# Optimization experiments

Measured on AMD Instinct MI355X. Metric: run time of the kernel, lower is better.

Reference implementation:

```python
import jax, jax.numpy as jnp
import numpy as np

PATCH = 3
PAD = (PATCH - 1) // 2
WEIGHT = 100.0
EPS = 1e-9


def _extract_patches(fm):
    # fm: (C, H, W) -> (H*W, C*9) row i*W+j is the reflect-padded 3x3 patch at (i, j)
    C, H, W = fm.shape
    fm_pad = jnp.pad(fm, ((0, 0), (PAD, PAD), (PAD, PAD)), mode='reflect')
    shifts = [fm_pad[:, dh:dh + H, dw:dw + W] for dh in range(PATCH) for dw in range(PATCH)]
    p = jnp.stack(shifts, axis=0)            # (9, C, H, W)
    return p.reshape(PATCH * PATCH * C, H * W).T  # (HW, 9C)


def _match_fm(content_fm, style_fm):
    # content_fm, style_fm: (1, C, H, W); returns matched style fm (1,C,H,W) and idx (2,H,W)
    C, H, W = content_fm.shape[1:]
    cp = _extract_patches(content_fm[0])     # (HW, 9C) content patches (conv kernels)
    sp = _extract_patches(style_fm[0])       # (HW, 9C) style patches (conv sliding windows)
    c_norm = jnp.sqrt(jnp.sum(cp * cp, axis=1))  # kernel_norm per content location
    s_norm = jnp.sqrt(jnp.sum(sp * sp, axis=1))  # style_fm_norm per style location
    score = cp @ sp.T                            # (HW, HW) cross-correlation
    score = score / (c_norm[:, None] * s_norm[None, :] + EPS)
    idx = jnp.argmax(score, axis=1)              # flat argmax == torch.argmax on (H,W) map
    style_flat = style_fm[0].reshape(C, H * W)
    corr = style_flat[:, idx].reshape(1, C, H, W)  # gather matched style pixels
    corr_idx = jnp.stack([idx // W, idx % W], axis=0).reshape(2, H, W)
    return corr, corr_idx


def _masked_gram(fm, mask_flat, mask_sum):
    # fm: (1, C, H, W), mask_flat: (HW,) -> (C, C) gram of masked fm / sum(mask)
    C = fm.shape[1]
    f = fm[0].reshape(C, -1) * mask_flat[None, :]
    return (f @ f.T) / mask_sum


def setup_inputs() -> dict:
    key = jax.random.key(0)
    k1, k2, k3, k4 = jax.random.split(key, 4)
    B, C, H, W = 1, 512, 64, 64
    return {
        'content_fm': jax.random.normal(k1, (B, C, H, W), dtype=jnp.float32),
        'style_fm': jax.random.normal(k2, (B, C, H, W), dtype=jnp.float32),
        'input_fm': jax.random.normal(k3, (B, C, H, W), dtype=jnp.float32),
        'mask': jax.random.uniform(k4, (B, 1, H, W), dtype=jnp.float32),
    }


def reference(content_fm, style_fm, input_fm, mask):
    H, W = content_fm.shape[2:]
    mask_flat = mask[0, 0].reshape(H * W)
    mask_sum = jnp.sum(mask)
    # capture_style_ref: patch-match style fm to content fm, build target gram
    corr_fm, _ = _match_fm(content_fm, style_fm)
    target_gram = _masked_gram(corr_fm, mask_flat, mask_sum)
    # loss mode: masked gram of current image fm vs target, MSE (mean) * weight
    G = _masked_gram(input_fm, mask_flat, mask_sum)
    loss = jnp.mean((G - target_gram) ** 2) * WEIGHT
    return loss
```

## Files before the change

kernel.cpp:

```cpp
#include <hip/hip_runtime.h>

static constexpr int C  = 512;
static constexpr int P  = 4096;
static constexpr int CC = 262144;

typedef _Float16 half8  __attribute__((ext_vector_type(8)));
typedef _Float16 half2v __attribute__((ext_vector_type(2)));
typedef float    f32x4  __attribute__((ext_vector_type(4)));

__device__ __forceinline__ int refl(int q) { return q < 0 ? 1 : (q > 63 ? 62 : q); }

__device__ __forceinline__ void g2l16(const void* g, const void* l) {
    __builtin_amdgcn_global_load_lds((const __attribute__((address_space(1))) unsigned int*)g,
                                     (__attribute__((address_space(3))) unsigned int*)l, 16, 0, 0);
}

__global__ void k_init(float* __restrict__ small) {
    int e = blockIdx.x * 256 + threadIdx.x;
    if (e < 4096) small[e] = 0.0f;
    if (e == 4096) small[8193] = 0.0f;
}

__global__ __launch_bounds__(256) void k_prep(const float* __restrict__ content, const float* __restrict__ style,
                                              _Float16* __restrict__ Ah, _Float16* __restrict__ Bh,
                                              float* __restrict__ sqn_s) {
    __shared__ float T[64][65];
    const int p0 = (blockIdx.x & 63) * 64, c0 = (blockIdx.x >> 6) * 64;
    const int pl = threadIdx.x & 63, cq = threadIdx.x >> 6;
    const int cl2 = threadIdx.x & 63, pq = threadIdx.x >> 6;

    #pragma unroll
    for (int r = 0; r < 16; ++r) {
        int cl = cq + r * 4;
        T[cl][pl] = content[(size_t)(c0 + cl) * P + p0 + pl];
    }
    __syncthreads();
    #pragma unroll
    for (int r = 0; r < 16; ++r) {
        int pl2 = pq + r * 4;
        Ah[(size_t)(p0 + pl2) * C + c0 + cl2] = (_Float16)T[cl2][pl2];
    }
    __syncthreads();

    float sq = 0.f;
    #pragma unroll
    for (int r = 0; r < 16; ++r) {
        int cl = cq + r * 4;
        float v = style[(size_t)(c0 + cl) * P + p0 + pl];
        T[cl][pl] = v;
        sq += v * v;
    }
    atomicAdd(&sqn_s[p0 + pl], sq);
    __syncthreads();
    #pragma unroll
    for (int r = 0; r < 16; ++r) {
        int pl2 = pq + r * 4;
        Bh[(size_t)(p0 + pl2) * C + c0 + cl2] = (_Float16)T[cl2][pl2];
    }
}

__global__ void k_pnorm(const float* __restrict__ sqn_s, const float* __restrict__ mask,
                        float* __restrict__ inv_sn, float* __restrict__ msum) {
    int p = blockIdx.x * 256 + threadIdx.x;
    int i = p >> 6, j = p & 63;
    float s2 = 0.f;
    #pragma unroll
    for (int dh = -1; dh <= 1; ++dh) {
        int ih = refl(i + dh);
        #pragma unroll
        for (int dw = -1; dw <= 1; ++dw)
            s2 += sqn_s[ih * 64 + refl(j + dw)];
    }
    inv_sn[p] = 1.0f / sqrtf(s2);

    if (blockIdx.x == 0) {
        __shared__ float red[256];
        float s = 0.f;
        for (int e = threadIdx.x; e < P; e += 256) s += mask[e];
        red[threadIdx.x] = s;
        __syncthreads();
        for (int t = 128; t > 0; t >>= 1) {
            if (threadIdx.x < t) red[threadIdx.x] += red[threadIdx.x + t];
            __syncthreads();
        }
        if (threadIdx.x == 0) msum[0] = red[0];
    }
}

__global__ __launch_bounds__(256) void k_gemm16(const _Float16* __restrict__ Ah,
                                                const _Float16* __restrict__ Bh,
                                                _Float16* __restrict__ D0h) {
    __shared__ _Float16 As[128 * 64];
    __shared__ _Float16 Bs[128 * 64];
    const int tid = threadIdx.x;
    const int wave = tid >> 6, lane = tid & 63;
    const int wr = wave >> 1, wc = wave & 1;
    const int quad = lane >> 4, l15 = lane & 15;
    const int i0 = blockIdx.y * 128, j0 = blockIdx.x * 128;

    int mloc[4], goff[4];
    #pragma unroll
    for (int c2 = 0; c2 < 4; ++c2) {
        int m = wave * 32 + c2 * 8 + (lane >> 3);
        mloc[c2] = m;
        goff[c2] = ((lane & 7) ^ (m & 7)) * 8;
    }

    int aoff[4][2], boff[4][2];
    #pragma unroll
    for (int mi = 0; mi < 4; ++mi) {
        int m = wr * 64 + mi * 16 + l15;
        int n = wc * 64 + mi * 16 + l15;
        #pragma unroll
        for (int kh = 0; kh < 2; ++kh) {
            aoff[mi][kh] = m * 64 + ((quad + kh * 4) ^ (m & 7)) * 8;
            boff[mi][kh] = n * 64 + ((quad + kh * 4) ^ (n & 7)) * 8;
        }
    }

    f32x4 acc[4][4] = {};

    for (int kk = 0; kk < C; kk += 64) {
        __syncthreads();
        #pragma unroll
        for (int c2 = 0; c2 < 4; ++c2) {
            g2l16(Ah + (size_t)(i0 + mloc[c2]) * C + kk + goff[c2], As + (wave * 32 + c2 * 8) * 64);
            g2l16(Bh + (size_t)(j0 + mloc[c2]) * C + kk + goff[c2], Bs + (wave * 32 + c2 * 8) * 64);
        }
        __syncthreads();
        half8 af[2][4], bf[2][4];
        #pragma unroll
        for (int kh = 0; kh < 2; ++kh)
            #pragma unroll
            for (int mi = 0; mi < 4; ++mi) {
                af[kh][mi] = *(const half8*)(As + aoff[mi][kh]);
                bf[kh][mi] = *(const half8*)(Bs + boff[mi][kh]);
            }
        #pragma unroll
        for (int kh = 0; kh < 2; ++kh)
            #pragma unroll
            for (int mi = 0; mi < 4; ++mi)
                #pragma unroll
                for (int ni = 0; ni < 4; ++ni)
                    acc[mi][ni] = __builtin_amdgcn_mfma_f32_16x16x32_f16(af[kh][mi], bf[kh][ni], acc[mi][ni], 0, 0, 0);
    }

    #pragma unroll
    for (int mi = 0; mi < 4; ++mi) {
        int row = i0 + wr * 64 + mi * 16 + quad * 4;
        #pragma unroll
        for (int ni = 0; ni < 4; ++ni) {
            int col = j0 + wc * 64 + ni * 16 + l15;
            #pragma unroll
            for (int r = 0; r < 4; ++r)
                D0h[(size_t)(row + r) * P + col] = (_Float16)acc[mi][ni][r];
        }
    }
}

__global__ __launch_bounds__(256) void k_argmax(const _Float16* __restrict__ D0h,
                                                const float* __restrict__ inv_sn,
                                                int* __restrict__ idxOut) {
    const int i = blockIdx.x;
    const int ih = i >> 6, iw = i & 63;
    const int wave = threadIdx.x >> 6, l = threadIdx.x & 63, l15 = l & 15;
    int rb[9];
    #pragma unroll
    for (int t = 0; t < 9; ++t) {
        int dh = t / 3 - 1, dw = t % 3 - 1;
        rb[t] = (refl(ih + dh) * 64 + refl(iw + dw)) * P;
    }
    float best = -1e30f;
    int bidx = 0;
    #pragma unroll
    for (int s = 0; s < 4; ++s) {
        const int ws = wave * 4 + s;
        const int j0 = ws * 256 + l * 4;
        const int jh = j0 >> 6;
        const int jw0 = l15 * 4;
        const int rs0 = (jh == 0) ? 1 : jh - 1;
        const int rs2 = (jh == 63) ? 62 : jh + 1;
        const int cb[3] = { rs0 * 64 + jw0, jh * 64 + jw0, rs2 * 64 + jw0 };

        float f[4] = {0.f, 0.f, 0.f, 0.f};
        #pragma unroll
        for (int dh = 0; dh < 3; ++dh) {
            const uint2 vm = *(const uint2*)(D0h + rb[dh * 3 + 0] + cb[dh]);
            const uint2 vc = *(const uint2*)(D0h + rb[dh * 3 + 1] + cb[dh]);
            const uint2 vp = *(const uint2*)(D0h + rb[dh * 3 + 2] + cb[dh]);
            unsigned prev_hi = (unsigned)__shfl((int)vm.y, l - 1);
            unsigned next_lo = (unsigned)__shfl((int)vp.x, l + 1);
            unsigned left16  = ((l15 == 0) ? vm.x : prev_hi) >> 16;
            unsigned right16 = ((l15 == 15) ? vp.y : next_lo) & 0xffffu;
            unsigned wl0 = left16 | (vm.x << 16);
            unsigned wl1 = (vm.x >> 16) | (vm.y << 16);
            unsigned wr0 = (vp.x >> 16) | (vp.y << 16);
            unsigned wr1 = (vp.y >> 16) | (right16 << 16);
            half2v a0 = __builtin_bit_cast(half2v, wl0), a1 = __builtin_bit_cast(half2v, wl1);
            half2v b0 = __builtin_bit_cast(half2v, vc.x), b1 = __builtin_bit_cast(half2v, vc.y);
            half2v c0 = __builtin_bit_cast(half2v, wr0), c1 = __builtin_bit_cast(half2v, wr1);
            f[0] += (float)a0[0] + (float)b0[0] + (float)c0[0];
            f[1] += (float)a0[1] + (float)b0[1] + (float)c0[1];
            f[2] += (float)a1[0] + (float)b1[0] + (float)c1[0];
            f[3] += (float)a1[1] + (float)b1[1] + (float)c1[1];
        }
        const float4 is = *(const float4*)(inv_sn + j0);
        float v0 = f[0] * is.x, v1 = f[1] * is.y, v2 = f[2] * is.z, v3 = f[3] * is.w;
        if (v0 > best) { best = v0; bidx = j0; }
        if (v1 > best) { best = v1; bidx = j0 + 1; }
        if (v2 > best) { best = v2; bidx = j0 + 2; }
        if (v3 > best) { best = v3; bidx = j0 + 3; }
    }
    __shared__ float bv[256];
    __shared__ int   bi[256];
    bv[threadIdx.x] = best;
    bi[threadIdx.x] = bidx;
    __syncthreads();
    for (int t = 128; t > 0; t >>= 1) {
        if (threadIdx.x < t) {
            float ov = bv[threadIdx.x + t];
            int   oi = bi[threadIdx.x + t];
            if (ov > bv[threadIdx.x] || (ov == bv[threadIdx.x] && oi < bi[threadIdx.x])) {
                bv[threadIdx.x] = ov;
                bi[threadIdx.x] = oi;
            }
        }
        __syncthreads();
    }
    if (threadIdx.x == 0) idxOut[i] = bi[0];
}

__global__ void k_build(const float* __restrict__ style, const float* __restrict__ input,
                        const float* __restrict__ mask, const int* __restrict__ idx,
                        _Float16* __restrict__ fc, _Float16* __restrict__ fg) {
    int t = blockIdx.x * 256 + threadIdx.x;
    int e0 = t * 8;
    int p0 = e0 & (P - 1), c = e0 >> 12;
    half8 vg, vc;
    #pragma unroll
    for (int u = 0; u < 8; ++u) {
        float m = mask[p0 + u];
        vg[u] = (_Float16)(input[e0 + u] * m);
        vc[u] = (_Float16)(style[(c << 12) + idx[p0 + u]] * m);
    }
    *(half8*)(fg + e0) = vg;
    *(half8*)(fc + e0) = vc;
}

__global__ __launch_bounds__(256) void k_gram(const _Float16* __restrict__ fg,
                                              const _Float16* __restrict__ fc,
                                              float* __restrict__ part) {
    const int z = blockIdx.z;
    const int p0 = z * 256;
    const int wave = threadIdx.x >> 6, lane = threadIdx.x & 63;
    const int wr = wave >> 1, wc = wave & 1, quad = lane >> 4, l15 = lane & 15;
    const int a0 = blockIdx.y * 128 + wr * 64, b0 = blockIdx.x * 128 + wc * 64;

    f32x4 accg[4][4] = {};
    f32x4 accc[4][4] = {};
    for (int ks = 0; ks < 256; ks += 32) {
        int kbase = p0 + ks + quad * 8;
        half8 af[4], bf[4];
        #pragma unroll
        for (int mi = 0; mi < 4; ++mi) af[mi] = *(const half8*)(fg + (size_t)(a0 + mi * 16 + l15) * P + kbase);
        #pragma unroll
        for (int ni = 0; ni < 4; ++ni) bf[ni] = *(const half8*)(fg + (size_t)(b0 + ni * 16 + l15) * P + kbase);
        #pragma unroll
        for (int mi = 0; mi < 4; ++mi)
            #pragma unroll
            for (int ni = 0; ni < 4; ++ni)
                accg[mi][ni] = __builtin_amdgcn_mfma_f32_16x16x32_f16(af[mi], bf[ni], accg[mi][ni], 0, 0, 0);
        #pragma unroll
        for (int mi = 0; mi < 4; ++mi) af[mi] = *(const half8*)(fc + (size_t)(a0 + mi * 16 + l15) * P + kbase);
        #pragma unroll
        for (int ni = 0; ni < 4; ++ni) bf[ni] = *(const half8*)(fc + (size_t)(b0 + ni * 16 + l15) * P + kbase);
        #pragma unroll
        for (int mi = 0; mi < 4; ++mi)
            #pragma unroll
            for (int ni = 0; ni < 4; ++ni)
                accc[mi][ni] = __builtin_amdgcn_mfma_f32_16x16x32_f16(af[mi], bf[ni], accc[mi][ni], 0, 0, 0);
    }
    #pragma unroll
    for (int mi = 0; mi < 4; ++mi)
        #pragma unroll
        for (int ni = 0; ni < 4; ++ni)
            #pragma unroll
            for (int r = 0; r < 4; ++r)
                part[(size_t)z * CC + (size_t)(a0 + mi * 16 + quad * 4 + r) * C + b0 + ni * 16 + l15]
                    = accg[mi][ni][r] - accc[mi][ni][r];
}

__global__ void k_loss(const float* __restrict__ part, float* __restrict__ acc) {
    int e = blockIdx.x * 256 + threadIdx.x;
    float d = 0.f;
    #pragma unroll
    for (int z = 0; z < 16; ++z) d += part[(size_t)z * CC + e];
    __shared__ float red[256];
    red[threadIdx.x] = d * d;
    __syncthreads();
    for (int t = 128; t > 0; t >>= 1) {
        if (threadIdx.x < t) red[threadIdx.x] += red[threadIdx.x + t];
        __syncthreads();
    }
    if (threadIdx.x == 0) atomicAdd(acc, red[0]);
}

__global__ void k_final(const float* __restrict__ msum, const float* __restrict__ acc,
                        float* __restrict__ out) {
    float m = msum[0];
    out[0] = acc[0] * 100.0f / (m * m * 262144.0f);
}

extern "C" void kernel_launch(void* const* d_in, const int* in_sizes, int n_in,
                              void* d_out, int out_size, void* d_ws, size_t ws_size,
                              hipStream_t stream) {
    (void)in_sizes; (void)n_in; (void)out_size; (void)ws_size;
    const float* content = (const float*)d_in[0];
    const float* style   = (const float*)d_in[1];
    const float* input   = (const float*)d_in[2];
    const float* mask    = (const float*)d_in[3];

    char* ws = (char*)d_ws;
    _Float16* D0h  = (_Float16*)ws;
    float*    part = (float*)ws;
    _Float16* Ah   = (_Float16*)(ws + (32u << 20));
    _Float16* Bh   = (_Float16*)(ws + (36u << 20));
    _Float16* fg_h = (_Float16*)(ws + (40u << 20));
    _Float16* fc_h = (_Float16*)(ws + (44u << 20));
    float*    small = (float*)(ws + (48u << 20));
    float* sqn_s  = small;
    float* inv_sn = small + 4096;
    float* msum   = small + 8192;
    float* acc    = small + 8193;
    int*   idx    = (int*)(small + 8194);
    float* out = (float*)d_out;

    k_init  <<<17, 256, 0, stream>>>(small);
    k_prep  <<<512, 256, 0, stream>>>(content, style, Ah, Bh, sqn_s);
    k_pnorm <<<16, 256, 0, stream>>>(sqn_s, mask, inv_sn, msum);
    k_gemm16<<<dim3(32, 32), 256, 0, stream>>>(Ah, Bh, D0h);
    k_argmax<<<4096, 256, 0, stream>>>(D0h, inv_sn, idx);
    k_build <<<1024, 256, 0, stream>>>(style, input, mask, idx, fc_h, fg_h);
    k_gram  <<<dim3(4, 4, 16), 256, 0, stream>>>(fg_h, fc_h, part);
    k_loss  <<<1024, 256, 0, stream>>>(part, acc);
    k_final <<<1, 1, 0, stream>>>(msum, acc, out);
}
```

Measured before the change: 173.8 us.

## Tile argmax over 2x2 content pixels and fold small kernels via last-block counters

```diff
diff --git a/kernel.cpp b/kernel.cpp
--- a/kernel.cpp
+++ b/kernel.cpp
@@ -15,15 +15,22 @@
                                      (__attribute__((address_space(3))) unsigned int*)l, 16, 0, 0);
 }
 
+
 __global__ void k_init(float* __restrict__ small) {
     int e = blockIdx.x * 256 + threadIdx.x;
     if (e < 4096) small[e] = 0.0f;
-    if (e == 4096) small[8193] = 0.0f;
+    if (e == 0) {
+        small[8193] = 0.0f;
+        ((unsigned*)small)[8194] = 0u;
+        ((unsigned*)small)[8195] = 0u;
+    }
 }
 
 __global__ __launch_bounds__(256) void k_prep(const float* __restrict__ content, const float* __restrict__ style,
+                                              const float* __restrict__ mask,
                                               _Float16* __restrict__ Ah, _Float16* __restrict__ Bh,
-                                              float* __restrict__ sqn_s) {
+                                              float* __restrict__ sqn_s, float* __restrict__ inv_sn,
+                                              float* __restrict__ msum, unsigned* __restrict__ cnt) {
     __shared__ float T[64][65];
     const int p0 = (blockIdx.x & 63) * 64, c0 = (blockIdx.x >> 6) * 64;
     const int pl = threadIdx.x & 63, cq = threadIdx.x >> 6;
@@ -57,26 +64,32 @@
         int pl2 = pq + r * 4;
         Bh[(size_t)(p0 + pl2) * C + c0 + cl2] = (_Float16)T[cl2][pl2];
     }
-}
-
-__global__ void k_pnorm(const float* __restrict__ sqn_s, const float* __restrict__ mask,
-                        float* __restrict__ inv_sn, float* __restrict__ msum) {
-    int p = blockIdx.x * 256 + threadIdx.x;
-    int i = p >> 6, j = p & 63;
-    float s2 = 0.f;
-    #pragma unroll
-    for (int dh = -1; dh <= 1; ++dh) {
-        int ih = refl(i + dh);
-        #pragma unroll
-        for (int dw = -1; dw <= 1; ++dw)
-            s2 += sqn_s[ih * 64 + refl(j + dw)];
-    }
-    inv_sn[p] = 1.0f / sqrtf(s2);
-
-    if (blockIdx.x == 0) {
+
+    __threadfence();
+    __syncthreads();
+    __shared__ unsigned lastv;
+    if (threadIdx.x == 0) lastv = atomicAdd(cnt, 1);
+    __syncthreads();
+    if (lastv == 511) {
+        __shared__ float sqs[4096];
+        for (int r = threadIdx.x; r < 4096; r += 256)
+            sqs[r] = __hip_atomic_load(&sqn_s[r], __ATOMIC_RELAXED, __HIP_MEMORY_SCOPE_AGENT);
+        __syncthreads();
+        for (int r = threadIdx.x; r < 4096; r += 256) {
+            int i = r >> 6, j = r & 63;
+            float s2 = 0.f;
+            #pragma unroll
+            for (int dh = -1; dh <= 1; ++dh) {
+                int ih = refl(i + dh);
+                #pragma unroll
+                for (int dw = -1; dw <= 1; ++dw)
+                    s2 += sqs[ih * 64 + refl(j + dw)];
+            }
+            inv_sn[r] = 1.0f / sqrtf(s2);
+        }
         __shared__ float red[256];
         float s = 0.f;
-        for (int e = threadIdx.x; e < P; e += 256) s += mask[e];
+        for (int e = threadIdx.x; e < 4096; e += 256) s += mask[e];
         red[threadIdx.x] = s;
         __syncthreads();
         for (int t = 128; t > 0; t >>= 1) {
@@ -161,17 +174,25 @@
 __global__ __launch_bounds__(256) void k_argmax(const _Float16* __restrict__ D0h,
                                                 const float* __restrict__ inv_sn,
                                                 int* __restrict__ idxOut) {
-    const int i = blockIdx.x;
-    const int ih = i >> 6, iw = i & 63;
+    const int T = blockIdx.x;
+    const int ih0 = (T >> 5) * 2, iw0 = (T & 31) * 2;
     const int wave = threadIdx.x >> 6, l = threadIdx.x & 63, l15 = l & 15;
-    int rb[9];
-    #pragma unroll
-    for (int t = 0; t < 9; ++t) {
-        int dh = t / 3 - 1, dw = t % 3 - 1;
-        rb[t] = (refl(ih + dh) * 64 + refl(iw + dw)) * P;
-    }
-    float best = -1e30f;
-    int bidx = 0;
+
+    int rh[4], rw[4];
+    rh[0] = refl(ih0 - 1); rh[1] = ih0; rh[2] = ih0 + 1; rh[3] = refl(ih0 + 2);
+    rw[0] = refl(iw0 - 1); rw[1] = iw0; rw[2] = iw0 + 1; rw[3] = refl(iw0 + 2);
+    int rb[3][2][4];
+    #pragma unroll
+    for (int d = 0; d < 3; ++d)
+        #pragma unroll
+        for (int di = 0; di < 2; ++di)
+            #pragma unroll
+            for (int k = 0; k < 4; ++k)
+                rb[d][di][k] = (rh[di + d] * 64 + rw[k]) * P;
+
+    float best[2][2] = {{-1e30f, -1e30f}, {-1e30f, -1e30f}};
+    int   bidx[2][2] = {{0, 0}, {0, 0}};
+
     #pragma unroll
     for (int s = 0; s < 4; ++s) {
         const int ws = wave * 4 + s;
@@ -182,52 +203,73 @@
         const int rs2 = (jh == 63) ? 62 : jh + 1;
         const int cb[3] = { rs0 * 64 + jw0, jh * 64 + jw0, rs2 * 64 + jw0 };
 
-        float f[4] = {0.f, 0.f, 0.f, 0.f};
-        #pragma unroll
-        for (int dh = 0; dh < 3; ++dh) {
-            const uint2 vm = *(const uint2*)(D0h + rb[dh * 3 + 0] + cb[dh]);
-            const uint2 vc = *(const uint2*)(D0h + rb[dh * 3 + 1] + cb[dh]);
-            const uint2 vp = *(const uint2*)(D0h + rb[dh * 3 + 2] + cb[dh]);
-            unsigned prev_hi = (unsigned)__shfl((int)vm.y, l - 1);
-            unsigned next_lo = (unsigned)__shfl((int)vp.x, l + 1);
-            unsigned left16  = ((l15 == 0) ? vm.x : prev_hi) >> 16;
-            unsigned right16 = ((l15 == 15) ? vp.y : next_lo) & 0xffffu;
-            unsigned wl0 = left16 | (vm.x << 16);
-            unsigned wl1 = (vm.x >> 16) | (vm.y << 16);
-            unsigned wr0 = (vp.x >> 16) | (vp.y << 16);
-            unsigned wr1 = (vp.y >> 16) | (right16 << 16);
-            half2v a0 = __builtin_bit_cast(half2v, wl0), a1 = __builtin_bit_cast(half2v, wl1);
-            half2v b0 = __builtin_bit_cast(half2v, vc.x), b1 = __builtin_bit_cast(half2v, vc.y);
-            half2v c0 = __builtin_bit_cast(half2v, wr0), c1 = __builtin_bit_cast(half2v, wr1);
-            f[0] += (float)a0[0] + (float)b0[0] + (float)c0[0];
-            f[1] += (float)a0[1] + (float)b0[1] + (float)c0[1];
-            f[2] += (float)a1[0] + (float)b1[0] + (float)c1[0];
-            f[3] += (float)a1[1] + (float)b1[1] + (float)c1[1];
+        float f[2][2][4] = {};
+        #pragma unroll
+        for (int d = 0; d < 3; ++d) {
+            #pragma unroll
+            for (int di = 0; di < 2; ++di) {
+                uint2 u[4];
+                #pragma unroll
+                for (int k = 0; k < 4; ++k)
+                    u[k] = *(const uint2*)(D0h + rb[d][di][k] + cb[d]);
+                #pragma unroll
+                for (int dj = 0; dj < 2; ++dj) {
+                    const uint2 A = u[dj], Bc = u[dj + 1], Cc = u[dj + 2];
+                    unsigned prev_hi = (unsigned)__shfl((int)A.y, l - 1);
+                    unsigned next_lo = (unsigned)__shfl((int)Cc.x, l + 1);
+                    unsigned left16  = ((l15 == 0) ? A.x : prev_hi) >> 16;
+                    unsigned right16 = ((l15 == 15) ? Cc.y : next_lo) & 0xffffu;
+                    unsigned wl0 = left16 | (A.x << 16);
+                    unsigned wl1 = (A.x >> 16) | (A.y << 16);
+                    unsigned wr0 = (Cc.x >> 16) | (Cc.y << 16);
+                    unsigned wr1 = (Cc.y >> 16) | (right16 << 16);
+                    half2v a0 = __builtin_bit_cast(half2v, wl0), a1 = __builtin_bit_cast(half2v, wl1);
+                    half2v b0 = __builtin_bit_cast(half2v, Bc.x), b1 = __builtin_bit_cast(half2v, Bc.y);
+                    half2v c0 = __builtin_bit_cast(half2v, wr0), c1 = __builtin_bit_cast(half2v, wr1);
+                    f[di][dj][0] += (float)a0[0] + (float)b0[0] + (float)c0[0];
+                    f[di][dj][1] += (float)a0[1] + (float)b0[1] + (float)c0[1];
+                    f[di][dj][2] += (float)a1[0] + (float)b1[0] + (float)c1[0];
+                    f[di][dj][3] += (float)a1[1] + (float)b1[1] + (float)c1[1];
+                }
+            }
         }
         const float4 is = *(const float4*)(inv_sn + j0);
-        float v0 = f[0] * is.x, v1 = f[1] * is.y, v2 = f[2] * is.z, v3 = f[3] * is.w;
-        if (v0 > best) { best = v0; bidx = j0; }
-        if (v1 > best) { best = v1; bidx = j0 + 1; }
-        if (v2 > best) { best = v2; bidx = j0 + 2; }
-        if (v3 > best) { best = v3; bidx = j0 + 3; }
-    }
+        #pragma unroll
+        for (int di = 0; di < 2; ++di)
+            #pragma unroll
+            for (int dj = 0; dj < 2; ++dj) {
+                float v0 = f[di][dj][0] * is.x, v1 = f[di][dj][1] * is.y;
+                float v2 = f[di][dj][2] * is.z, v3 = f[di][dj][3] * is.w;
+                if (v0 > best[di][dj]) { best[di][dj] = v0; bidx[di][dj] = j0; }
+                if (v1 > best[di][dj]) { best[di][dj] = v1; bidx[di][dj] = j0 + 1; }
+                if (v2 > best[di][dj]) { best[di][dj] = v2; bidx[di][dj] = j0 + 2; }
+                if (v3 > best[di][dj]) { best[di][dj] = v3; bidx[di][dj] = j0 + 3; }
+            }
+    }
+
     __shared__ float bv[256];
     __shared__ int   bi[256];
-    bv[threadIdx.x] = best;
-    bi[threadIdx.x] = bidx;
-    __syncthreads();
-    for (int t = 128; t > 0; t >>= 1) {
-        if (threadIdx.x < t) {
-            float ov = bv[threadIdx.x + t];
-            int   oi = bi[threadIdx.x + t];
-            if (ov > bv[threadIdx.x] || (ov == bv[threadIdx.x] && oi < bi[threadIdx.x])) {
-                bv[threadIdx.x] = ov;
-                bi[threadIdx.x] = oi;
-            }
-        }
-        __syncthreads();
-    }
-    if (threadIdx.x == 0) idxOut[i] = bi[0];
+    #pragma unroll
+    for (int di = 0; di < 2; ++di)
+        #pragma unroll
+        for (int dj = 0; dj < 2; ++dj) {
+            __syncthreads();
+            bv[threadIdx.x] = best[di][dj];
+            bi[threadIdx.x] = bidx[di][dj];
+            __syncthreads();
+            for (int t = 128; t > 0; t >>= 1) {
+                if (threadIdx.x < t) {
+                    float ov = bv[threadIdx.x + t];
+                    int   oi = bi[threadIdx.x + t];
+                    if (ov > bv[threadIdx.x] || (ov == bv[threadIdx.x] && oi < bi[threadIdx.x])) {
+                        bv[threadIdx.x] = ov;
+                        bi[threadIdx.x] = oi;
+                    }
+                }
+                __syncthreads();
+            }
+            if (threadIdx.x == 0) idxOut[(ih0 + di) * 64 + iw0 + dj] = bi[0];
+        }
 }
 
 __global__ void k_build(const float* __restrict__ style, const float* __restrict__ input,
@@ -290,7 +332,9 @@
                     = accg[mi][ni][r] - accc[mi][ni][r];
 }
 
-__global__ void k_loss(const float* __restrict__ part, float* __restrict__ acc) {
+__global__ void k_loss(const float* __restrict__ part, float* __restrict__ acc,
+                       unsigned* __restrict__ cnt, const float* __restrict__ msum,
+                       float* __restrict__ out) {
     int e = blockIdx.x * 256 + threadIdx.x;
     float d = 0.f;
     #pragma unroll
@@ -302,13 +346,16 @@
         if (threadIdx.x < t) red[threadIdx.x] += red[threadIdx.x + t];
         __syncthreads();
     }
-    if (threadIdx.x == 0) atomicAdd(acc, red[0]);
-}
-
-__global__ void k_final(const float* __restrict__ msum, const float* __restrict__ acc,
-                        float* __restrict__ out) {
-    float m = msum[0];
-    out[0] = acc[0] * 100.0f / (m * m * 262144.0f);
+    if (threadIdx.x == 0) {
+        atomicAdd(acc, red[0]);
+        __threadfence();
+        unsigned old = atomicAdd(cnt, 1);
+        if (old == 1023) {
+            float a = __hip_atomic_load(acc, __ATOMIC_RELAXED, __HIP_MEMORY_SCOPE_AGENT);
+            float m = msum[0];
+            out[0] = a * 100.0f / (m * m * 262144.0f);
+        }
+    }
 }
 
 extern "C" void kernel_launch(void* const* d_in, const int* in_sizes, int n_in,
@@ -328,20 +375,20 @@
     _Float16* fg_h = (_Float16*)(ws + (40u << 20));
     _Float16* fc_h = (_Float16*)(ws + (44u << 20));
     float*    small = (float*)(ws + (48u << 20));
-    float* sqn_s  = small;
-    float* inv_sn = small + 4096;
-    float* msum   = small + 8192;
-    float* acc    = small + 8193;
-    int*   idx    = (int*)(small + 8194);
+    float*    sqn_s  = small;
+    float*    inv_sn = small + 4096;
+    float*    msum   = small + 8192;
+    float*    acc    = small + 8193;
+    unsigned* cntp   = (unsigned*)(small + 8194);
+    unsigned* cntl   = (unsigned*)(small + 8195);
+    int*      idx    = (int*)(small + 8196);
     float* out = (float*)d_out;
 
-    k_init  <<<17, 256, 0, stream>>>(small);
-    k_prep  <<<512, 256, 0, stream>>>(content, style, Ah, Bh, sqn_s);
-    k_pnorm <<<16, 256, 0, stream>>>(sqn_s, mask, inv_sn, msum);
+    k_init  <<<16, 256, 0, stream>>>(small);
+    k_prep  <<<512, 256, 0, stream>>>(content, style, mask, Ah, Bh, sqn_s, inv_sn, msum, cntp);
     k_gemm16<<<dim3(32, 32), 256, 0, stream>>>(Ah, Bh, D0h);
-    k_argmax<<<4096, 256, 0, stream>>>(D0h, inv_sn, idx);
+    k_argmax<<<1024, 256, 0, stream>>>(D0h, inv_sn, idx);
     k_build <<<1024, 256, 0, stream>>>(style, input, mask, idx, fc_h, fg_h);
     k_gram  <<<dim3(4, 4, 16), 256, 0, stream>>>(fg_h, fc_h, part);
-    k_loss  <<<1024, 256, 0, stream>>>(part, acc);
-    k_final <<<1, 1, 0, stream>>>(msum, acc, out);
-}
+    k_loss  <<<1024, 256, 0, stream>>>(part, acc, cntl, msum, out);
+}
```

New measurement: 259.4 us. 1.49x slower.

## Fuse horizontal 3-tap patch sum into GEMM epilogue, simplify argmax to 3 taps

Applied to the files above, without the earlier changes.

```diff
diff --git a/kernel.cpp b/kernel.cpp
--- a/kernel.cpp
+++ b/kernel.cpp
@@ -18,7 +18,7 @@
 __global__ void k_init(float* __restrict__ small) {
     int e = blockIdx.x * 256 + threadIdx.x;
     if (e < 4096) small[e] = 0.0f;
-    if (e == 4096) small[8193] = 0.0f;
+    if (e == 0) small[8193] = 0.0f;
 }
 
 __global__ __launch_bounds__(256) void k_prep(const float* __restrict__ content, const float* __restrict__ style,
@@ -89,9 +89,10 @@
 
 __global__ __launch_bounds__(256) void k_gemm16(const _Float16* __restrict__ Ah,
                                                 const _Float16* __restrict__ Bh,
-                                                _Float16* __restrict__ D0h) {
-    __shared__ _Float16 As[128 * 64];
-    __shared__ _Float16 Bs[128 * 64];
+                                                _Float16* __restrict__ Eo) {
+    __shared__ _Float16 SH[16640];
+    _Float16* As = SH;
+    _Float16* Bs = SH + 8192;
     const int tid = threadIdx.x;
     const int wave = tid >> 6, lane = tid & 63;
     const int wr = wave >> 1, wc = wave & 1;
@@ -145,72 +146,78 @@
                     acc[mi][ni] = __builtin_amdgcn_mfma_f32_16x16x32_f16(af[kh][mi], bf[kh][ni], acc[mi][ni], 0, 0, 0);
     }
 
+    __syncthreads();
     #pragma unroll
     for (int mi = 0; mi < 4; ++mi) {
-        int row = i0 + wr * 64 + mi * 16 + quad * 4;
+        int row = wr * 64 + mi * 16 + quad * 4;
         #pragma unroll
         for (int ni = 0; ni < 4; ++ni) {
-            int col = j0 + wc * 64 + ni * 16 + l15;
+            int col = wc * 64 + ni * 16 + l15;
             #pragma unroll
             for (int r = 0; r < 4; ++r)
-                D0h[(size_t)(row + r) * P + col] = (_Float16)acc[mi][ni][r];
-        }
-    }
-}
-
-__global__ __launch_bounds__(256) void k_argmax(const _Float16* __restrict__ D0h,
+                SH[(row + r) * 130 + col] = (_Float16)acc[mi][ni][r];
+        }
+    }
+    __syncthreads();
+
+    const int er  = tid >> 1;
+    const int ec0 = (tid & 1) << 6;
+    const int aw = er & 63;
+    const int rm = (er & 64) | (aw == 0 ? 1 : aw - 1);
+    const int rp = (er & 64) | (aw == 63 ? 62 : aw + 1);
+    _Float16* outRow = Eo + (size_t)(i0 + er) * P + j0 + ec0;
+    #pragma unroll
+    for (int cc = 0; cc < 64; cc += 8) {
+        half8 ev;
+        #pragma unroll
+        for (int u = 0; u < 8; ++u) {
+            int c = ec0 + cc + u;
+            int cw = c & 63;
+            int cm = (c & 64) | (cw == 0 ? 1 : cw - 1);
+            int cp = (c & 64) | (cw == 63 ? 62 : cw + 1);
+            ev[u] = (_Float16)((float)SH[rm * 130 + cm] + (float)SH[er * 130 + c] + (float)SH[rp * 130 + cp]);
+        }
+        *(half8*)(outRow + cc) = ev;
+    }
+}
+
+__global__ __launch_bounds__(256) void k_argmax(const _Float16* __restrict__ E,
                                                 const float* __restrict__ inv_sn,
                                                 int* __restrict__ idxOut) {
     const int i = blockIdx.x;
     const int ih = i >> 6, iw = i & 63;
     const int wave = threadIdx.x >> 6, l = threadIdx.x & 63, l15 = l & 15;
-    int rb[9];
-    #pragma unroll
-    for (int t = 0; t < 9; ++t) {
-        int dh = t / 3 - 1, dw = t % 3 - 1;
-        rb[t] = (refl(ih + dh) * 64 + refl(iw + dw)) * P;
-    }
+    size_t rb0 = (size_t)(refl(ih - 1) * 64 + iw) * P;
+    size_t rb1 = (size_t)(ih * 64 + iw) * P;
+    size_t rb2 = (size_t)(refl(ih + 1) * 64 + iw) * P;
+
     float best = -1e30f;
     int bidx = 0;
     #pragma unroll
     for (int s = 0; s < 4; ++s) {
-        const int ws = wave * 4 + s;
-        const int j0 = ws * 256 + l * 4;
-        const int jh = j0 >> 6;
-        const int jw0 = l15 * 4;
-        const int rs0 = (jh == 0) ? 1 : jh - 1;
-        const int rs2 = (jh == 63) ? 62 : jh + 1;
-        const int cb[3] = { rs0 * 64 + jw0, jh * 64 + jw0, rs2 * 64 + jw0 };
-
-        float f[4] = {0.f, 0.f, 0.f, 0.f};
-        #pragma unroll
-        for (int dh = 0; dh < 3; ++dh) {
-            const uint2 vm = *(const uint2*)(D0h + rb[dh * 3 + 0] + cb[dh]);
-            const uint2 vc = *(const uint2*)(D0h + rb[dh * 3 + 1] + cb[dh]);
-            const uint2 vp = *(const uint2*)(D0h + rb[dh * 3 + 2] + cb[dh]);
-            unsigned prev_hi = (unsigned)__shfl((int)vm.y, l - 1);
-            unsigned next_lo = (unsigned)__shfl((int)vp.x, l + 1);
-            unsigned left16  = ((l15 == 0) ? vm.x : prev_hi) >> 16;
-            unsigned right16 = ((l15 == 15) ? vp.y : next_lo) & 0xffffu;
-            unsigned wl0 = left16 | (vm.x << 16);
-            unsigned wl1 = (vm.x >> 16) | (vm.y << 16);
-            unsigned wr0 = (vp.x >> 16) | (vp.y << 16);
-            unsigned wr1 = (vp.y >> 16) | (right16 << 16);
-            half2v a0 = __builtin_bit_cast(half2v, wl0), a1 = __builtin_bit_cast(half2v, wl1);
-            half2v b0 = __builtin_bit_cast(half2v, vc.x), b1 = __builtin_bit_cast(half2v, vc.y);
-            half2v c0 = __builtin_bit_cast(half2v, wr0), c1 = __builtin_bit_cast(half2v, wr1);
-            f[0] += (float)a0[0] + (float)b0[0] + (float)c0[0];
-            f[1] += (float)a0[1] + (float)b0[1] + (float)c0[1];
-            f[2] += (float)a1[0] + (float)b1[0] + (float)c1[0];
-            f[3] += (float)a1[1] + (float)b1[1] + (float)c1[1];
-        }
+        const int j0 = (wave * 4 + s) * 256 + l * 4;
+        const int jh = j0 >> 6, jw0 = l15 * 4;
+        const int cb0 = ((jh == 0) ? 1 : jh - 1) * 64 + jw0;
+        const int cb1 = jh * 64 + jw0;
+        const int cb2 = ((jh == 63) ? 62 : jh + 1) * 64 + jw0;
+        uint2 u0 = *(const uint2*)(E + rb0 + cb0);
+        uint2 u1 = *(const uint2*)(E + rb1 + cb1);
+        uint2 u2 = *(const uint2*)(E + rb2 + cb2);
+        half2v a0 = __builtin_bit_cast(half2v, u0.x), a1 = __builtin_bit_cast(half2v, u0.y);
+        half2v b0 = __builtin_bit_cast(half2v, u1.x), b1 = __builtin_bit_cast(half2v, u1.y);
+        half2v c0 = __builtin_bit_cast(half2v, u2.x), c1 = __builtin_bit_cast(half2v, u2.y);
+        float f0 = (float)a0[0] + (float)b0[0] + (float)c0[0];
+        float f1 = (float)a0[1] + (float)b0[1] + (float)c0[1];
+        float f2 = (float)a1[0] + (float)b1[0] + (float)c1[0];
+        float f3 = (float)a1[1] + (float)b1[1] + (float)c1[1];
         const float4 is = *(const float4*)(inv_sn + j0);
-        float v0 = f[0] * is.x, v1 = f[1] * is.y, v2 = f[2] * is.z, v3 = f[3] * is.w;
+        float v0 = f0 * is.x, v1 = f1 * is.y, v2 = f2 * is.z, v3 = f3 * is.w;
         if (v0 > best) { best = v0; bidx = j0; }
         if (v1 > best) { best = v1; bidx = j0 + 1; }
         if (v2 > best) { best = v2; bidx = j0 + 2; }
         if (v3 > best) { best = v3; bidx = j0 + 3; }
     }
+
     __shared__ float bv[256];
     __shared__ int   bi[256];
     bv[threadIdx.x] = best;
@@ -321,7 +328,7 @@
     const float* mask    = (const float*)d_in[3];
 
     char* ws = (char*)d_ws;
-    _Float16* D0h  = (_Float16*)ws;
+    _Float16* Eb   = (_Float16*)ws;
     float*    part = (float*)ws;
     _Float16* Ah   = (_Float16*)(ws + (32u << 20));
     _Float16* Bh   = (_Float16*)(ws + (36u << 20));
@@ -335,11 +342,11 @@
     int*   idx    = (int*)(small + 8194);
     float* out = (float*)d_out;
 
-    k_init  <<<17, 256, 0, stream>>>(small);
+    k_init  <<<16, 256, 0, stream>>>(small);
     k_prep  <<<512, 256, 0, stream>>>(content, style, Ah, Bh, sqn_s);
     k_pnorm <<<16, 256, 0, stream>>>(sqn_s, mask, inv_sn, msum);
-    k_gemm16<<<dim3(32, 32), 256, 0, stream>>>(Ah, Bh, D0h);
-    k_argmax<<<4096, 256, 0, stream>>>(D0h, inv_sn, idx);
+    k_gemm16<<<dim3(32, 32), 256, 0, stream>>>(Ah, Bh, Eb);
+    k_argmax<<<4096, 256, 0, stream>>>(Eb, inv_sn, idx);
     k_build <<<1024, 256, 0, stream>>>(style, input, mask, idx, fc_h, fg_h);
     k_gram  <<<dim3(4, 4, 16), 256, 0, stream>>>(fg_h, fc_h, part);
     k_loss  <<<1024, 256, 0, stream>>>(part, acc);
```

New measurement: 173.1 us. About the same (-0.4%).
